# Kernel optimization log

Hardware: AMD Instinct MI355X
Metric: run time of the kernel (lower is better)

Reference implementation:

```python
import jax, jax.numpy as jnp
import numpy as np

EMB = 1024
NH = 8
HD = EMB // NH
EPS = 1e-6


def setup_inputs() -> dict:
    key = jax.random.key(0)
    ks = jax.random.split(key, 6)
    B, S = 2, 2048
    q = jax.random.normal(ks[0], (B, S, EMB), jnp.float32)
    k = jax.random.normal(ks[1], (B, S, EMB), jnp.float32)
    v = jax.random.normal(ks[2], (B, S, EMB), jnp.float32)
    # gate Dense params: input dim 3*EMB (concat of q,k,v), output NH
    igate_kernel = jax.random.normal(ks[3], (3 * EMB, NH), jnp.float32) * 0.02
    igate_bias = jax.random.normal(ks[4], (NH,), jnp.float32) * 0.1
    fgate_kernel = jax.random.normal(ks[5], (3 * EMB, NH), jnp.float32) * 0.02
    fgate_bias = jnp.linspace(3.0, 6.0, NH).astype(jnp.float32)  # bias_linspace_init
    return dict(q=q, k=k, v=v, igate_kernel=igate_kernel, igate_bias=igate_bias,
                fgate_kernel=fgate_kernel, fgate_bias=fgate_bias)


def _mlstm_head(q, k, v, ig, fg):
    # q,k,v: (S, DH); ig, fg: (S, 1) gate preactivations for this head
    S, DH = q.shape
    log_fg = jax.nn.log_sigmoid(fg)                                   # (S,1)
    cs = jnp.concatenate([jnp.zeros((1, 1), q.dtype),
                          jnp.cumsum(log_fg, axis=0)], axis=0)        # (S+1,1)
    fg_mat_full = cs - cs.T                                           # (S+1,S+1): cumsum_i - cumsum_j
    ltr = jnp.tril(jnp.ones((S, S), bool))
    log_fg_matrix = jnp.where(ltr, fg_mat_full[1:, 1:], -jnp.inf)     # causal decay
    log_D = log_fg_matrix + ig.T                                      # (S,S)
    max_log_D = jnp.max(log_D, axis=-1, keepdims=True)                # row-wise stabilizer
    D = jnp.exp(log_D - max_log_D)
    qk = q @ (k.T / jnp.sqrt(jnp.asarray(DH, q.dtype)))               # (S,S)
    C = qk * D
    normalizer = jnp.maximum(jnp.abs(C.sum(-1, keepdims=True)), jnp.exp(-max_log_D))
    return (C / (normalizer + EPS)) @ v                               # (S,DH)


def reference(q, k, v, igate_kernel, igate_bias, fgate_kernel, fgate_bias):
    B, S, H = q.shape
    x = jnp.concatenate([q, k, v], axis=-1)                           # (B,S,3H)
    ig = x @ igate_kernel + igate_bias                                # (B,S,NH)
    fg = x @ fgate_kernel + fgate_bias                                # (B,S,NH)
    qh = q.reshape(B, S, NH, HD).swapaxes(1, 2)                       # (B,NH,S,DH)
    kh = k.reshape(B, S, NH, HD).swapaxes(1, 2)
    vh = v.reshape(B, S, NH, HD).swapaxes(1, 2)
    igp = ig.swapaxes(1, 2)[..., None]                                # (B,NH,S,1)
    fgp = fg.swapaxes(1, 2)[..., None]
    h = jax.vmap(jax.vmap(_mlstm_head))(qh, kh, vh, igp, fgp)         # (B,NH,S,DH)
    # RMSNorm over head_dim (last axis), computed in fp32
    hf = h.astype(jnp.float32)
    h = (hf * jax.lax.rsqrt(jnp.mean(jnp.square(hf), axis=-1, keepdims=True) + 1e-6)).astype(h.dtype)
    return h.swapaxes(1, 2).reshape(B, S, H)
```

## Files before the change

kernel.cpp:

```cpp
#include <hip/hip_runtime.h>

#define S_LEN 2048
#define EMB_D 1024
#define QK_SCALE 0.08838834764831845f
#define RS128 11.313708498984761f
#define LOG2E 1.4426950408889634f

typedef _Float16 f16;
typedef f16 f16x8 __attribute__((ext_vector_type(8)));
typedef float f32x4 __attribute__((ext_vector_type(4)));
typedef unsigned short ushort_t;

typedef const __attribute__((address_space(1))) void gvoid;
typedef __attribute__((address_space(3))) void lvoid;

__device__ __forceinline__ ushort_t f2h(float x) {
    return __builtin_bit_cast(ushort_t, (f16)x);
}
__device__ __forceinline__ unsigned pk2h(float a, float b) {
    return __builtin_bit_cast(unsigned, __builtin_amdgcn_cvt_pkrtz(a, b));
}
__device__ __forceinline__ void gl_lds(const void* g, void* l) {
    __builtin_amdgcn_global_load_lds((gvoid*)g, (lvoid*)l, 16, 0, 0);
}

__global__ __launch_bounds__(256) void ktransW(const float* __restrict__ igk,
                                               const float* __restrict__ fgk,
                                               ushort_t* __restrict__ Wf) {
    int gid = blockIdx.x * 256 + threadIdx.x;
    int ks_g = gid >> 6, lane = gid & 63;
    int n = lane & 15, lg = lane >> 4;
    int src = ks_g >> 5, rem = ks_g & 31;
    int hemb = rem >> 2, ks = rem & 3;
    int e0 = src * 1024 + hemb * 128 + ks * 32 + lg * 8;
    float scale = (src == 0) ? RS128 : 1.0f;
    const float* col = (n < 8) ? igk : fgk;
    int nn = n & 7;
    union { ushort_t u[8]; uint4 v4; } P;
    #pragma unroll
    for (int e = 0; e < 8; ++e) P.u[e] = f2h(col[(size_t)(e0 + e) * 8 + nn] * scale);
    *(uint4*)((char*)Wf + ks_g * 1024 + lane * 16) = P.v4;
}

__global__ __launch_bounds__(256) void kprep(const float* __restrict__ q,
                                             const float* __restrict__ k,
                                             const float* __restrict__ v,
                                             const ushort_t* __restrict__ Wf,
                                             const float* __restrict__ igb,
                                             const float* __restrict__ fgb,
                                             ushort_t* __restrict__ Qf,
                                             ushort_t* __restrict__ Kf,
                                             ushort_t* __restrict__ Vt,
                                             float* __restrict__ igp_t,
                                             float* __restrict__ fgp_t) {
    __shared__ __align__(16) ushort_t xs[3 * 8 * 16 * 128];
    __shared__ __align__(16) float red[4][64][4];
    const int blk = blockIdx.x;
    const int b = blk >> 7, strip = blk & 127;
    const int s0 = strip * 16;
    const int tile = strip >> 2, subrow = (strip & 3) * 16;
    const int t = threadIdx.x;
    const int w = t >> 6, lane = t & 63;
    const int ll = lane & 15, lg = lane >> 4;

    #pragma unroll
    for (int src = 0; src < 3; ++src) {
        const float* sp = (src == 0 ? q : src == 1 ? k : v) + ((size_t)b * S_LEN + s0) * EMB_D;
        float scale = (src == 0) ? QK_SCALE : 1.0f;
        #pragma unroll
        for (int i = 0; i < 16; ++i) {
            int f = i * 256 + t;
            int r = f >> 8, c4 = f & 255;
            int col = c4 * 4;
            float4 x = *(const float4*)(sp + (size_t)r * EMB_D + col);
            ushort4 H;
            H.x = f2h(x.x * scale); H.y = f2h(x.y * scale);
            H.z = f2h(x.z * scale); H.w = f2h(x.w * scale);
            int hh = col >> 7, d0 = col & 127;
            *(ushort4*)((char*)xs + ((((src * 8 + hh) * 16 + r) * 256 + d0 * 2) ^ ((r & 7) << 4))) = H;
            if (src < 2) {
                char* dst = (char*)(src ? Kf : Qf) + ((size_t)(b * 8 + hh) * 32 + tile) * 16384;
                *(ushort4*)(dst + (((subrow + r) * 256 + d0 * 2) ^ ((r & 7) << 4))) = H;
            }
        }
    }
    __syncthreads();
    #pragma unroll
    for (int it = 0; it < 8; ++it) {
        int item = it * 256 + t;
        int d = item & 127, jo = (item >> 7) & 1, hh = item >> 8;
        union { ushort_t u[8]; uint4 v4; } P;
        #pragma unroll
        for (int e = 0; e < 8; ++e) {
            int r = jo * 8 + e;
            P.u[e] = *(const ushort_t*)((const char*)xs
                       + ((((16 + hh) * 16 + r) * 256 + d * 2) ^ ((r & 7) << 4)));
        }
        char* vd = (char*)Vt + ((size_t)(b * 8 + hh) * 32 + tile) * 16384
                 + ((strip & 3) * 2 + jo) * 2048 + d * 16;
        *(uint4*)vd = P.v4;
    }
    f32x4 acc = {0.f, 0.f, 0.f, 0.f};
    for (int ri = w * 6; ri < w * 6 + 6; ++ri) {
        int src = ri >> 3, hemb = ri & 7;
        #pragma unroll
        for (int ks = 0; ks < 4; ++ks) {
            f16x8 af = *(const f16x8*)((const char*)xs
                        + ((((src * 8 + hemb) * 16 + ll) * 256 + ks * 64 + lg * 16) ^ ((ll & 7) << 4)));
            f16x8 bf = *(const f16x8*)((const char*)Wf + (src * 32 + hemb * 4 + ks) * 1024 + lane * 16);
            acc = __builtin_amdgcn_mfma_f32_16x16x32_f16(af, bf, acc, 0, 0, 0);
        }
    }
    *(f32x4*)&red[w][lane][0] = acc;
    __syncthreads();
    if (w == 0) {
        f32x4 o2 = acc;
        #pragma unroll
        for (int ww = 1; ww < 4; ++ww) o2 += *(const f32x4*)&red[ww][lane][0];
        float bias = (ll < 8) ? igb[ll] : fgb[ll - 8];
        float* dst = (ll < 8) ? igp_t : fgp_t;
        size_t ob = (size_t)(b * 8 + (ll & 7)) * S_LEN + s0 + lg * 4;
        #pragma unroll
        for (int r = 0; r < 4; ++r) dst[ob + r] = o2[r] + bias;
    }
}

__global__ __launch_bounds__(64) void kscan(const float* __restrict__ igp_t,
                                            const float* __restrict__ fgp_t,
                                            float* __restrict__ a_w,
                                            float* __restrict__ pm_w,
                                            float* __restrict__ nf_w) {
    const int bh = blockIdx.x;
    const int l = threadIdx.x;
    const int base = bh * S_LEN + l * 32;
    float lf[32];
    #pragma unroll
    for (int i = 0; i < 8; ++i) {
        float4 fg = *(const float4*)(fgp_t + base + i * 4);
        float* p = &lf[i * 4];
        p[0] = fminf(fg.x, 0.f) - log1pf(__expf(-fabsf(fg.x)));
        p[1] = fminf(fg.y, 0.f) - log1pf(__expf(-fabsf(fg.y)));
        p[2] = fminf(fg.z, 0.f) - log1pf(__expf(-fabsf(fg.z)));
        p[3] = fminf(fg.w, 0.f) - log1pf(__expf(-fabsf(fg.w)));
    }
    #pragma unroll
    for (int i = 1; i < 32; ++i) lf[i] += lf[i - 1];
    float tot = lf[31];
    #pragma unroll
    for (int d = 1; d < 64; d <<= 1) {
        float n = __shfl_up(tot, d, 64);
        if (l >= d) tot += n;
    }
    float excl = tot - lf[31];
    float cs[32], a[32];
    #pragma unroll
    for (int i = 0; i < 8; ++i) {
        float4 ig = *(const float4*)(igp_t + base + i * 4);
        float iv[4] = {ig.x, ig.y, ig.z, ig.w};
        #pragma unroll
        for (int e = 0; e < 4; ++e) {
            int idx = i * 4 + e;
            cs[idx] = excl + lf[idx];
            a[idx] = iv[e] - cs[idx];
            a_w[base + idx] = a[idx] * LOG2E;
        }
    }
    float am[32];
    am[0] = a[0];
    #pragma unroll
    for (int i = 1; i < 32; ++i) am[i] = fmaxf(am[i - 1], a[i]);
    float mtot = am[31];
    #pragma unroll
    for (int d = 1; d < 64; d <<= 1) {
        float n = __shfl_up(mtot, d, 64);
        if (l >= d) mtot = fmaxf(mtot, n);
    }
    float exm = __shfl_up(mtot, 1, 64);
    if (l == 0) exm = -INFINITY;
    #pragma unroll
    for (int i = 0; i < 32; ++i) {
        float pmv = fmaxf(exm, am[i]);
        pm_w[base + i] = pmv * LOG2E;
        nf_w[base + i] = __expf(-(cs[i] + pmv));
    }
}

__global__ __launch_bounds__(512) void kmain(const ushort_t* __restrict__ Qf,
                                             const ushort_t* __restrict__ Kf,
                                             const ushort_t* __restrict__ Vt,
                                             const float* __restrict__ a_w,
                                             const float* __restrict__ pm_w,
                                             const float* __restrict__ nf_w,
                                             float* __restrict__ out) {
    __shared__ __align__(16) ushort_t Kbuf[2][2][8192];
    __shared__ __align__(16) ushort_t Vbuf[2][2][8192];
    __shared__ __align__(16) ushort_t Csh[2][4096];
    __shared__ float redL[2][2][64];

    const int blk = blockIdx.x;
    const int bh = blk & 15;
    const int pair = blk >> 4;
    const int b = bh >> 3, h = bh & 7;
    const int t = threadIdx.x;
    const int w = t >> 6, lane = t & 63;
    const int g = w >> 2, wl = w & 3;
    const int wr = wl >> 1, wc = wl & 1;
    const int lg = lane >> 4, ll = lane & 15;
    const int sw = (ll & 7) << 4;

    const char* q_b = (const char*)Qf + (size_t)bh * 524288;
    const char* k_b = (const char*)Kf + (size_t)bh * 524288;
    const char* v_b = (const char*)Vt + (size_t)bh * 524288;
    const float* aw = a_w + bh * S_LEN;

    float* accX = (float*)&Kbuf[0][0][0];
    float* rsX  = (float*)&Csh[0][0];

    for (int half = 0; half < 2; ++half) {
        const int rt = half ? (31 - pair) : pair;
        const int row0 = rt * 64;
        const int T0h = (rt >> 1) + 1;
        const int T1h = (rt >= 1) ? (((rt - 1) >> 1) + 1) : 0;
        const int Tg  = g ? T1h : T0h;
        const int Nint = (2 * T1h + 1 > 2 * T0h) ? (2 * T1h + 1) : (2 * T0h);
        __syncthreads();

        const char* qt = q_b + (size_t)rt * 16384;
        f16x8 qf[2][4];
        #pragma unroll
        for (int ib = 0; ib < 2; ++ib) {
            int row = 32 * wr + 16 * ib + ll;
            #pragma unroll
            for (int kk = 0; kk < 4; ++kk)
                qf[ib][kk] = *(const f16x8*)(qt + ((row * 256 + lg * 16 + kk * 64) ^ ((row & 7) << 4)));
        }
        float pm2[2];
        #pragma unroll
        for (int ib = 0; ib < 2; ++ib)
            pm2[ib] = pm_w[bh * S_LEN + row0 + 32 * wr + 16 * ib + ll];

        f32x4 avA[2] = {{0.f,0.f,0.f,0.f},{0.f,0.f,0.f,0.f}};
        f32x4 avB[2] = {{0.f,0.f,0.f,0.f},{0.f,0.f,0.f,0.f}};
        if (Tg > 0) {
            const char* kt = k_b + (size_t)g * 16384;
            const char* vt = v_b + (size_t)g * 16384;
            #pragma unroll
            for (int i = 0; i < 4; ++i) {
                int o = (wl * 4 + i) * 1024 + lane * 16;
                gl_lds(kt + o, (char*)&Kbuf[g][0][0] + o);
                gl_lds(vt + o, (char*)&Vbuf[g][0][0] + o);
            }
            #pragma unroll
            for (int jb = 0; jb < 2; ++jb)
                avA[jb] = *(const f32x4*)(aw + g * 64 + 32 * wc + 16 * jb + 4 * lg);
        }
        asm volatile("s_waitcnt vmcnt(0)" ::: "memory");
        __builtin_amdgcn_s_barrier();

        f32x4 zero4 = {0.f, 0.f, 0.f, 0.f};
        f32x4 accO[2][4];
        #pragma unroll
        for (int ib = 0; ib < 2; ++ib)
            #pragma unroll
            for (int vf = 0; vf < 4; ++vf) accO[ib][vf] = zero4;
        float rs[2] = {0.f, 0.f};

        for (int i = 0; i < Nint; ++i) {
            const int d = i - g;
            const bool isQK = (d >= 0) && ((d & 1) == 0) && ((d >> 1) < Tg);
            const bool isPV = (d >= 1) && ((d & 1) == 1) && (((d - 1) >> 1) < Tg);
            if (isQK) {
                const int tt = d >> 1;
                const int ct = 2 * tt + g;
                if (tt + 1 < Tg) {
                    const int nct = ct + 2;
                    const char* kt = k_b + (size_t)nct * 16384;
                    const char* vt = v_b + (size_t)nct * 16384;
                    const int pn = (tt + 1) & 1;
                    #pragma unroll
                    for (int ii = 0; ii < 4; ++ii) {
                        int o = (wl * 4 + ii) * 1024 + lane * 16;
                        gl_lds(kt + o, (char*)&Kbuf[g][pn][0] + o);
                        gl_lds(vt + o, (char*)&Vbuf[g][pn][0] + o);
                    }
                    if ((tt + 1) & 1) {
                        #pragma unroll
                        for (int jb = 0; jb < 2; ++jb)
                            avB[jb] = *(const f32x4*)(aw + nct * 64 + 32 * wc + 16 * jb + 4 * lg);
                    } else {
                        #pragma unroll
                        for (int jb = 0; jb < 2; ++jb)
                            avA[jb] = *(const f32x4*)(aw + nct * 64 + 32 * wc + 16 * jb + 4 * lg);
                    }
                }
                const char* kl = (const char*)&Kbuf[g][tt & 1][0];
                f32x4 accST[2][2];
                accST[0][0] = zero4; accST[0][1] = zero4;
                accST[1][0] = zero4; accST[1][1] = zero4;
                __builtin_amdgcn_s_setprio(1);
                #pragma unroll
                for (int kk = 0; kk < 4; ++kk) {
                    f16x8 kf0 = *(const f16x8*)(kl + (((32 * wc + ll) * 256 + lg * 16 + kk * 64) ^ sw));
                    f16x8 kf1 = *(const f16x8*)(kl + (((32 * wc + 16 + ll) * 256 + lg * 16 + kk * 64) ^ sw));
                    accST[0][0] = __builtin_amdgcn_mfma_f32_16x16x32_f16(kf0, qf[0][kk], accST[0][0], 0, 0, 0);
                    accST[0][1] = __builtin_amdgcn_mfma_f32_16x16x32_f16(kf0, qf[1][kk], accST[0][1], 0, 0, 0);
                    accST[1][0] = __builtin_amdgcn_mfma_f32_16x16x32_f16(kf1, qf[0][kk], accST[1][0], 0, 0, 0);
                    accST[1][1] = __builtin_amdgcn_mfma_f32_16x16x32_f16(kf1, qf[1][kk], accST[1][1], 0, 0, 0);
                }
                __builtin_amdgcn_s_setprio(0);
                const bool diag = (ct == rt);
                #pragma unroll
                for (int jb = 0; jb < 2; ++jb) {
                    f32x4 av;
                    #pragma unroll
                    for (int r = 0; r < 4; ++r) av[r] = (tt & 1) ? avB[jb][r] : avA[jb][r];
                    #pragma unroll
                    for (int ib = 0; ib < 2; ++ib) {
                        int il = 32 * wr + 16 * ib + ll;
                        float cv[4];
                        #pragma unroll
                        for (int r = 0; r < 4; ++r) {
                            int jl = 32 * wc + 16 * jb + 4 * lg + r;
                            float x = accST[jb][ib][r] * exp2f(av[r] - pm2[ib]);
                            if (diag && jl > il) x = 0.f;
                            rs[ib] += x;
                            cv[r] = x;
                        }
                        int off = (il * 128 + (32 * wc + 16 * jb + 4 * lg) * 2) ^ ((il & 7) << 4);
                        uint2 pk2; pk2.x = pk2h(cv[0], cv[1]); pk2.y = pk2h(cv[2], cv[3]);
                        *(uint2*)((char*)&Csh[g][0] + off) = pk2;
                    }
                }
                asm volatile("s_waitcnt lgkmcnt(0)" ::: "memory");
            }
            if (isPV) {
                const int tp = (d - 1) >> 1;
                const char* vl = (const char*)&Vbuf[g][tp & 1][0];
                __builtin_amdgcn_s_setprio(1);
                #pragma unroll
                for (int kk = 0; kk < 2; ++kk)
                    #pragma unroll
                    for (int ib = 0; ib < 2; ++ib) {
                        int rowA = 32 * wr + 16 * ib + ll;
                        f16x8 pa = *(const f16x8*)((const char*)&Csh[g][0]
                                                   + ((rowA * 128 + lg * 16 + kk * 64) ^ ((rowA & 7) << 4)));
                        #pragma unroll
                        for (int vf = 0; vf < 4; ++vf) {
                            f16x8 vb2 = *(const f16x8*)(vl + (kk * 4 + lg) * 2048
                                                        + (64 * wc + 16 * vf + ll) * 16);
                            accO[ib][vf] = __builtin_amdgcn_mfma_f32_16x16x32_f16(pa, vb2, accO[ib][vf], 0, 0, 0);
                        }
                    }
                __builtin_amdgcn_s_setprio(0);
                asm volatile("s_waitcnt vmcnt(0)" ::: "memory");
            }
            __builtin_amdgcn_s_barrier();
        }

        __syncthreads();
        const int li = wl * 64 + lane;
        const int lsw = (li & 7) << 2;
        if (g == 1) {
            #pragma unroll
            for (int ib = 0; ib < 2; ++ib)
                #pragma unroll
                for (int vf = 0; vf < 4; ++vf)
                    *(f32x4*)&accX[(li * 32 + (ib * 4 + vf) * 4) ^ lsw] = accO[ib][vf];
            rsX[li * 2 + 0] = rs[0];
            rsX[li * 2 + 1] = rs[1];
        }
        __syncthreads();
        if (g == 0) {
            #pragma unroll
            for (int ib = 0; ib < 2; ++ib)
                #pragma unroll
                for (int vf = 0; vf < 4; ++vf)
                    accO[ib][vf] += *(const f32x4*)&accX[(li * 32 + (ib * 4 + vf) * 4) ^ lsw];
            rs[0] += rsX[li * 2 + 0];
            rs[1] += rsX[li * 2 + 1];
            #pragma unroll
            for (int ib = 0; ib < 2; ++ib) {
                rs[ib] += __shfl_xor(rs[ib], 16);
                rs[ib] += __shfl_xor(rs[ib], 32);
            }
            if (lg == 0) {
                redL[0][wc][32 * wr + ll] = rs[0];
                redL[0][wc][32 * wr + 16 + ll] = rs[1];
            }
        }
        __syncthreads();
        if (g == 0) {
            float invn[2][4];
            #pragma unroll
            for (int ib = 0; ib < 2; ++ib)
                #pragma unroll
                for (int r = 0; r < 4; ++r) {
                    int il = 32 * wr + 16 * ib + 4 * lg + r;
                    float tot = redL[0][0][il] + redL[0][1][il];
                    float nf = nf_w[bh * S_LEN + row0 + il];
                    invn[ib][r] = 1.0f / (fmaxf(fabsf(tot), nf) + 1e-6f);
                }
            float ssq[2][4] = {{0.f, 0.f, 0.f, 0.f}, {0.f, 0.f, 0.f, 0.f}};
            #pragma unroll
            for (int ib = 0; ib < 2; ++ib)
                #pragma unroll
                for (int vf = 0; vf < 4; ++vf)
                    #pragma unroll
                    for (int r = 0; r < 4; ++r) {
                        float hv = accO[ib][vf][r] * invn[ib][r];
                        ssq[ib][r] += hv * hv;
                    }
            #pragma unroll
            for (int m = 1; m < 16; m <<= 1)
                #pragma unroll
                for (int ib = 0; ib < 2; ++ib)
                    #pragma unroll
                    for (int r = 0; r < 4; ++r) ssq[ib][r] += __shfl_xor(ssq[ib][r], m);
            if (ll == 0) {
                #pragma unroll
                for (int ib = 0; ib < 2; ++ib)
                    #pragma unroll
                    for (int r = 0; r < 4; ++r)
                        redL[1][wc][32 * wr + 16 * ib + 4 * lg + r] = ssq[ib][r];
            }
            __builtin_amdgcn_s_barrier();
            float* ob = out + ((size_t)b * S_LEN + row0) * EMB_D + h * 128;
            #pragma unroll
            for (int ib = 0; ib < 2; ++ib)
                #pragma unroll
                for (int r = 0; r < 4; ++r) {
                    int il = 32 * wr + 16 * ib + 4 * lg + r;
                    float sst = redL[1][0][il] + redL[1][1][il];
                    float scl = rsqrtf(sst * (1.0f / 128.0f) + 1e-6f) * invn[ib][r];
                    #pragma unroll
                    for (int vf = 0; vf < 4; ++vf) {
                        int d2 = 64 * wc + 16 * vf + ll;
                        ob[(size_t)il * EMB_D + d2] = accO[ib][vf][r] * scl;
                    }
                }
        } else {
            __builtin_amdgcn_s_barrier();
        }
    }
}

extern "C" void kernel_launch(void* const* d_in, const int* in_sizes, int n_in,
                              void* d_out, int out_size, void* d_ws, size_t ws_size,
                              hipStream_t stream) {
    const float* q   = (const float*)d_in[0];
    const float* k   = (const float*)d_in[1];
    const float* v   = (const float*)d_in[2];
    const float* igk = (const float*)d_in[3];
    const float* igb = (const float*)d_in[4];
    const float* fgk = (const float*)d_in[5];
    const float* fgb = (const float*)d_in[6];
    float* out = (float*)d_out;

    char* W = (char*)d_ws;
    ushort_t* Wf   = (ushort_t*)(W);
    float* igp_t   = (float*)(W + 98304);
    float* fgp_t   = (float*)(W + 229376);
    float* a_w     = (float*)(W + 360448);
    float* pm_w    = (float*)(W + 491520);
    float* nf_w    = (float*)(W + 622592);
    ushort_t* Qf   = (ushort_t*)(W + 753664);
    ushort_t* Kf   = (ushort_t*)(W + 753664 + 1 * 8388608ull);
    ushort_t* Vt   = (ushort_t*)(W + 753664 + 2 * 8388608ull);

    ktransW<<<24, 256, 0, stream>>>(igk, fgk, Wf);
    kprep<<<256, 256, 0, stream>>>(q, k, v, Wf, igb, fgb, Qf, Kf, Vt, igp_t, fgp_t);
    kscan<<<16, 64, 0, stream>>>(igp_t, fgp_t, a_w, pm_w, nf_w);
    kmain<<<256, 512, 0, stream>>>(Qf, Kf, Vt, a_w, pm_w, nf_w, out);
}
```

Measured before the change: 90.76 us.

## Split kmain into one row tile per block without key-split groups

Replaces the two-group key-split, staggered QK/PV pipeline (512-thread blocks each processing two row tiles) with 256-thread blocks that each handle a single row tile over all causal key tiles. This removes the cross-group accumulator reduction through LDS and halves shared memory per block, and launches twice as many blocks with heavy tiles scheduled first. In exchange it loses the intra-block overlap of one group's QK with the other's PV, and the longest rows now run a longer serial chain per block.

```diff
diff --git a/kernel.cpp b/kernel.cpp
--- a/kernel.cpp
+++ b/kernel.cpp
@@ -185,26 +185,27 @@
     }
 }
 
-__global__ __launch_bounds__(512) void kmain(const ushort_t* __restrict__ Qf,
+__global__ __launch_bounds__(256) void kmain(const ushort_t* __restrict__ Qf,
                                              const ushort_t* __restrict__ Kf,
                                              const ushort_t* __restrict__ Vt,
                                              const float* __restrict__ a_w,
                                              const float* __restrict__ pm_w,
                                              const float* __restrict__ nf_w,
                                              float* __restrict__ out) {
-    __shared__ __align__(16) ushort_t Kbuf[2][2][8192];
-    __shared__ __align__(16) ushort_t Vbuf[2][2][8192];
-    __shared__ __align__(16) ushort_t Csh[2][4096];
+    __shared__ __align__(16) ushort_t Kbuf[2][8192];
+    __shared__ __align__(16) ushort_t Vbuf[2][8192];
+    __shared__ __align__(16) ushort_t Csh[4096];
     __shared__ float redL[2][2][64];
 
     const int blk = blockIdx.x;
     const int bh = blk & 15;
-    const int pair = blk >> 4;
+    const int jj = (blk >> 4) & 15;
+    const int rt = (blk < 256) ? (31 - jj) : jj;
+    const int row0 = rt * 64;
     const int b = bh >> 3, h = bh & 7;
     const int t = threadIdx.x;
     const int w = t >> 6, lane = t & 63;
-    const int g = w >> 2, wl = w & 3;
-    const int wr = wl >> 1, wc = wl & 1;
+    const int wr = w >> 1, wc = w & 1;
     const int lg = lane >> 4, ll = lane & 15;
     const int sw = (ll & 7) << 4;
 
@@ -213,235 +214,189 @@
     const char* v_b = (const char*)Vt + (size_t)bh * 524288;
     const float* aw = a_w + bh * S_LEN;
 
-    float* accX = (float*)&Kbuf[0][0][0];
-    float* rsX  = (float*)&Csh[0][0];
-
-    for (int half = 0; half < 2; ++half) {
-        const int rt = half ? (31 - pair) : pair;
-        const int row0 = rt * 64;
-        const int T0h = (rt >> 1) + 1;
-        const int T1h = (rt >= 1) ? (((rt - 1) >> 1) + 1) : 0;
-        const int Tg  = g ? T1h : T0h;
-        const int Nint = (2 * T1h + 1 > 2 * T0h) ? (2 * T1h + 1) : (2 * T0h);
-        __syncthreads();
-
-        const char* qt = q_b + (size_t)rt * 16384;
-        f16x8 qf[2][4];
-        #pragma unroll
-        for (int ib = 0; ib < 2; ++ib) {
-            int row = 32 * wr + 16 * ib + ll;
-            #pragma unroll
-            for (int kk = 0; kk < 4; ++kk)
-                qf[ib][kk] = *(const f16x8*)(qt + ((row * 256 + lg * 16 + kk * 64) ^ ((row & 7) << 4)));
-        }
-        float pm2[2];
-        #pragma unroll
-        for (int ib = 0; ib < 2; ++ib)
-            pm2[ib] = pm_w[bh * S_LEN + row0 + 32 * wr + 16 * ib + ll];
-
-        f32x4 avA[2] = {{0.f,0.f,0.f,0.f},{0.f,0.f,0.f,0.f}};
-        f32x4 avB[2] = {{0.f,0.f,0.f,0.f},{0.f,0.f,0.f,0.f}};
-        if (Tg > 0) {
-            const char* kt = k_b + (size_t)g * 16384;
-            const char* vt = v_b + (size_t)g * 16384;
+    const char* qt = q_b + (size_t)rt * 16384;
+    f16x8 qf[2][4];
+    #pragma unroll
+    for (int ib = 0; ib < 2; ++ib) {
+        int row = 32 * wr + 16 * ib + ll;
+        #pragma unroll
+        for (int kk = 0; kk < 4; ++kk)
+            qf[ib][kk] = *(const f16x8*)(qt + ((row * 256 + lg * 16 + kk * 64) ^ ((row & 7) << 4)));
+    }
+    float pm2[2];
+    #pragma unroll
+    for (int ib = 0; ib < 2; ++ib)
+        pm2[ib] = pm_w[bh * S_LEN + row0 + 32 * wr + 16 * ib + ll];
+
+    f32x4 avA[2], avB[2];
+    {
+        const char* kt = k_b;
+        const char* vt = v_b;
+        #pragma unroll
+        for (int i = 0; i < 4; ++i) {
+            int o = (w * 4 + i) * 1024 + lane * 16;
+            gl_lds(kt + o, (char*)&Kbuf[0][0] + o);
+            gl_lds(vt + o, (char*)&Vbuf[0][0] + o);
+        }
+        #pragma unroll
+        for (int jb = 0; jb < 2; ++jb)
+            avA[jb] = *(const f32x4*)(aw + 32 * wc + 16 * jb + 4 * lg);
+        avB[0] = avA[0]; avB[1] = avA[1];
+    }
+    asm volatile("s_waitcnt vmcnt(0)" ::: "memory");
+    __builtin_amdgcn_s_barrier();
+
+    f32x4 zero4 = {0.f, 0.f, 0.f, 0.f};
+    f32x4 accO[2][4];
+    #pragma unroll
+    for (int ib = 0; ib < 2; ++ib)
+        #pragma unroll
+        for (int vf = 0; vf < 4; ++vf) accO[ib][vf] = zero4;
+    float rs[2] = {0.f, 0.f};
+
+    for (int ct = 0; ct <= rt; ++ct) {
+        const int p = ct & 1;
+        if (ct < rt) {
+            const int nct = ct + 1;
+            const char* kt = k_b + (size_t)nct * 16384;
+            const char* vt = v_b + (size_t)nct * 16384;
             #pragma unroll
             for (int i = 0; i < 4; ++i) {
-                int o = (wl * 4 + i) * 1024 + lane * 16;
-                gl_lds(kt + o, (char*)&Kbuf[g][0][0] + o);
-                gl_lds(vt + o, (char*)&Vbuf[g][0][0] + o);
-            }
-            #pragma unroll
-            for (int jb = 0; jb < 2; ++jb)
-                avA[jb] = *(const f32x4*)(aw + g * 64 + 32 * wc + 16 * jb + 4 * lg);
+                int o = (w * 4 + i) * 1024 + lane * 16;
+                gl_lds(kt + o, (char*)&Kbuf[p ^ 1][0] + o);
+                gl_lds(vt + o, (char*)&Vbuf[p ^ 1][0] + o);
+            }
+            if (p == 0) {
+                #pragma unroll
+                for (int jb = 0; jb < 2; ++jb)
+                    avB[jb] = *(const f32x4*)(aw + nct * 64 + 32 * wc + 16 * jb + 4 * lg);
+            } else {
+                #pragma unroll
+                for (int jb = 0; jb < 2; ++jb)
+                    avA[jb] = *(const f32x4*)(aw + nct * 64 + 32 * wc + 16 * jb + 4 * lg);
+            }
+        }
+        const char* kl = (const char*)&Kbuf[p][0];
+        f32x4 accST[2][2];
+        accST[0][0] = zero4; accST[0][1] = zero4;
+        accST[1][0] = zero4; accST[1][1] = zero4;
+        __builtin_amdgcn_s_setprio(1);
+        #pragma unroll
+        for (int kk = 0; kk < 4; ++kk) {
+            f16x8 kf0 = *(const f16x8*)(kl + (((32 * wc + ll) * 256 + lg * 16 + kk * 64) ^ sw));
+            f16x8 kf1 = *(const f16x8*)(kl + (((32 * wc + 16 + ll) * 256 + lg * 16 + kk * 64) ^ sw));
+            accST[0][0] = __builtin_amdgcn_mfma_f32_16x16x32_f16(kf0, qf[0][kk], accST[0][0], 0, 0, 0);
+            accST[0][1] = __builtin_amdgcn_mfma_f32_16x16x32_f16(kf0, qf[1][kk], accST[0][1], 0, 0, 0);
+            accST[1][0] = __builtin_amdgcn_mfma_f32_16x16x32_f16(kf1, qf[0][kk], accST[1][0], 0, 0, 0);
+            accST[1][1] = __builtin_amdgcn_mfma_f32_16x16x32_f16(kf1, qf[1][kk], accST[1][1], 0, 0, 0);
+        }
+        __builtin_amdgcn_s_setprio(0);
+        const bool diag = (ct == rt);
+        #pragma unroll
+        for (int jb = 0; jb < 2; ++jb) {
+            f32x4 av;
+            #pragma unroll
+            for (int r = 0; r < 4; ++r) av[r] = (p == 0) ? avA[jb][r] : avB[jb][r];
+            #pragma unroll
+            for (int ib = 0; ib < 2; ++ib) {
+                int il = 32 * wr + 16 * ib + ll;
+                float cv[4];
+                #pragma unroll
+                for (int r = 0; r < 4; ++r) {
+                    int jl = 32 * wc + 16 * jb + 4 * lg + r;
+                    float x = accST[jb][ib][r] * exp2f(av[r] - pm2[ib]);
+                    if (diag && jl > il) x = 0.f;
+                    rs[ib] += x;
+                    cv[r] = x;
+                }
+                int off = (il * 128 + (32 * wc + 16 * jb + 4 * lg) * 2) ^ ((il & 7) << 4);
+                uint2 pk2; pk2.x = pk2h(cv[0], cv[1]); pk2.y = pk2h(cv[2], cv[3]);
+                *(uint2*)((char*)&Csh[0] + off) = pk2;
+            }
+        }
+        asm volatile("s_waitcnt lgkmcnt(0)" ::: "memory");
+        __builtin_amdgcn_s_barrier();
+        {
+            const char* vl = (const char*)&Vbuf[p][0];
+            __builtin_amdgcn_s_setprio(1);
+            #pragma unroll
+            for (int kk = 0; kk < 2; ++kk)
+                #pragma unroll
+                for (int ib = 0; ib < 2; ++ib) {
+                    int rowA = 32 * wr + 16 * ib + ll;
+                    f16x8 pa = *(const f16x8*)((const char*)&Csh[0]
+                                               + ((rowA * 128 + lg * 16 + kk * 64) ^ ((rowA & 7) << 4)));
+                    #pragma unroll
+                    for (int vf = 0; vf < 4; ++vf) {
+                        f16x8 vb2 = *(const f16x8*)(vl + (kk * 4 + lg) * 2048
+                                                    + (64 * wc + 16 * vf + ll) * 16);
+                        accO[ib][vf] = __builtin_amdgcn_mfma_f32_16x16x32_f16(pa, vb2, accO[ib][vf], 0, 0, 0);
+                    }
+                }
+            __builtin_amdgcn_s_setprio(0);
         }
         asm volatile("s_waitcnt vmcnt(0)" ::: "memory");
         __builtin_amdgcn_s_barrier();
-
-        f32x4 zero4 = {0.f, 0.f, 0.f, 0.f};
-        f32x4 accO[2][4];
+    }
+
+    #pragma unroll
+    for (int ib = 0; ib < 2; ++ib) {
+        rs[ib] += __shfl_xor(rs[ib], 16);
+        rs[ib] += __shfl_xor(rs[ib], 32);
+    }
+    if (lg == 0) {
+        redL[0][wc][32 * wr + ll] = rs[0];
+        redL[0][wc][32 * wr + 16 + ll] = rs[1];
+    }
+    __syncthreads();
+    float invn[2][4];
+    #pragma unroll
+    for (int ib = 0; ib < 2; ++ib)
+        #pragma unroll
+        for (int r = 0; r < 4; ++r) {
+            int il = 32 * wr + 16 * ib + 4 * lg + r;
+            float tot = redL[0][0][il] + redL[0][1][il];
+            float nf = nf_w[bh * S_LEN + row0 + il];
+            invn[ib][r] = 1.0f / (fmaxf(fabsf(tot), nf) + 1e-6f);
+        }
+    float ssq[2][4] = {{0.f, 0.f, 0.f, 0.f}, {0.f, 0.f, 0.f, 0.f}};
+    #pragma unroll
+    for (int ib = 0; ib < 2; ++ib)
+        #pragma unroll
+        for (int vf = 0; vf < 4; ++vf)
+            #pragma unroll
+            for (int r = 0; r < 4; ++r) {
+                float hv = accO[ib][vf][r] * invn[ib][r];
+                ssq[ib][r] += hv * hv;
+            }
+    #pragma unroll
+    for (int m = 1; m < 16; m <<= 1)
         #pragma unroll
         for (int ib = 0; ib < 2; ++ib)
             #pragma unroll
-            for (int vf = 0; vf < 4; ++vf) accO[ib][vf] = zero4;
-        float rs[2] = {0.f, 0.f};
-
-        for (int i = 0; i < Nint; ++i) {
-            const int d = i - g;
-            const bool isQK = (d >= 0) && ((d & 1) == 0) && ((d >> 1) < Tg);
-            const bool isPV = (d >= 1) && ((d & 1) == 1) && (((d - 1) >> 1) < Tg);
-            if (isQK) {
-                const int tt = d >> 1;
-                const int ct = 2 * tt + g;
-                if (tt + 1 < Tg) {
-                    const int nct = ct + 2;
-                    const char* kt = k_b + (size_t)nct * 16384;
-                    const char* vt = v_b + (size_t)nct * 16384;
-                    const int pn = (tt + 1) & 1;
-                    #pragma unroll
-                    for (int ii = 0; ii < 4; ++ii) {
-                        int o = (wl * 4 + ii) * 1024 + lane * 16;
-                        gl_lds(kt + o, (char*)&Kbuf[g][pn][0] + o);
-                        gl_lds(vt + o, (char*)&Vbuf[g][pn][0] + o);
-                    }
-                    if ((tt + 1) & 1) {
-                        #pragma unroll
-                        for (int jb = 0; jb < 2; ++jb)
-                            avB[jb] = *(const f32x4*)(aw + nct * 64 + 32 * wc + 16 * jb + 4 * lg);
-                    } else {
-                        #pragma unroll
-                        for (int jb = 0; jb < 2; ++jb)
-                            avA[jb] = *(const f32x4*)(aw + nct * 64 + 32 * wc + 16 * jb + 4 * lg);
-                    }
-                }
-                const char* kl = (const char*)&Kbuf[g][tt & 1][0];
-                f32x4 accST[2][2];
-                accST[0][0] = zero4; accST[0][1] = zero4;
-                accST[1][0] = zero4; accST[1][1] = zero4;
-                __builtin_amdgcn_s_setprio(1);
-                #pragma unroll
-                for (int kk = 0; kk < 4; ++kk) {
-                    f16x8 kf0 = *(const f16x8*)(kl + (((32 * wc + ll) * 256 + lg * 16 + kk * 64) ^ sw));
-                    f16x8 kf1 = *(const f16x8*)(kl + (((32 * wc + 16 + ll) * 256 + lg * 16 + kk * 64) ^ sw));
-                    accST[0][0] = __builtin_amdgcn_mfma_f32_16x16x32_f16(kf0, qf[0][kk], accST[0][0], 0, 0, 0);
-                    accST[0][1] = __builtin_amdgcn_mfma_f32_16x16x32_f16(kf0, qf[1][kk], accST[0][1], 0, 0, 0);
-                    accST[1][0] = __builtin_amdgcn_mfma_f32_16x16x32_f16(kf1, qf[0][kk], accST[1][0], 0, 0, 0);
-                    accST[1][1] = __builtin_amdgcn_mfma_f32_16x16x32_f16(kf1, qf[1][kk], accST[1][1], 0, 0, 0);
-                }
-                __builtin_amdgcn_s_setprio(0);
-                const bool diag = (ct == rt);
-                #pragma unroll
-                for (int jb = 0; jb < 2; ++jb) {
-                    f32x4 av;
-                    #pragma unroll
-                    for (int r = 0; r < 4; ++r) av[r] = (tt & 1) ? avB[jb][r] : avA[jb][r];
-                    #pragma unroll
-                    for (int ib = 0; ib < 2; ++ib) {
-                        int il = 32 * wr + 16 * ib + ll;
-                        float cv[4];
-                        #pragma unroll
-                        for (int r = 0; r < 4; ++r) {
-                            int jl = 32 * wc + 16 * jb + 4 * lg + r;
-                            float x = accST[jb][ib][r] * exp2f(av[r] - pm2[ib]);
-                            if (diag && jl > il) x = 0.f;
-                            rs[ib] += x;
-                            cv[r] = x;
-                        }
-                        int off = (il * 128 + (32 * wc + 16 * jb + 4 * lg) * 2) ^ ((il & 7) << 4);
-                        uint2 pk2; pk2.x = pk2h(cv[0], cv[1]); pk2.y = pk2h(cv[2], cv[3]);
-                        *(uint2*)((char*)&Csh[g][0] + off) = pk2;
-                    }
-                }
-                asm volatile("s_waitcnt lgkmcnt(0)" ::: "memory");
-            }
-            if (isPV) {
-                const int tp = (d - 1) >> 1;
-                const char* vl = (const char*)&Vbuf[g][tp & 1][0];
-                __builtin_amdgcn_s_setprio(1);
-                #pragma unroll
-                for (int kk = 0; kk < 2; ++kk)
-                    #pragma unroll
-                    for (int ib = 0; ib < 2; ++ib) {
-                        int rowA = 32 * wr + 16 * ib + ll;
-                        f16x8 pa = *(const f16x8*)((const char*)&Csh[g][0]
-                                                   + ((rowA * 128 + lg * 16 + kk * 64) ^ ((rowA & 7) << 4)));
-                        #pragma unroll
-                        for (int vf = 0; vf < 4; ++vf) {
-                            f16x8 vb2 = *(const f16x8*)(vl + (kk * 4 + lg) * 2048
-                                                        + (64 * wc + 16 * vf + ll) * 16);
-                            accO[ib][vf] = __builtin_amdgcn_mfma_f32_16x16x32_f16(pa, vb2, accO[ib][vf], 0, 0, 0);
-                        }
-                    }
-                __builtin_amdgcn_s_setprio(0);
-                asm volatile("s_waitcnt vmcnt(0)" ::: "memory");
-            }
-            __builtin_amdgcn_s_barrier();
-        }
-
-        __syncthreads();
-        const int li = wl * 64 + lane;
-        const int lsw = (li & 7) << 2;
-        if (g == 1) {
-            #pragma unroll
-            for (int ib = 0; ib < 2; ++ib)
-                #pragma unroll
-                for (int vf = 0; vf < 4; ++vf)
-                    *(f32x4*)&accX[(li * 32 + (ib * 4 + vf) * 4) ^ lsw] = accO[ib][vf];
-            rsX[li * 2 + 0] = rs[0];
-            rsX[li * 2 + 1] = rs[1];
-        }
-        __syncthreads();
-        if (g == 0) {
-            #pragma unroll
-            for (int ib = 0; ib < 2; ++ib)
-                #pragma unroll
-                for (int vf = 0; vf < 4; ++vf)
-                    accO[ib][vf] += *(const f32x4*)&accX[(li * 32 + (ib * 4 + vf) * 4) ^ lsw];
-            rs[0] += rsX[li * 2 + 0];
-            rs[1] += rsX[li * 2 + 1];
-            #pragma unroll
-            for (int ib = 0; ib < 2; ++ib) {
-                rs[ib] += __shfl_xor(rs[ib], 16);
-                rs[ib] += __shfl_xor(rs[ib], 32);
-            }
-            if (lg == 0) {
-                redL[0][wc][32 * wr + ll] = rs[0];
-                redL[0][wc][32 * wr + 16 + ll] = rs[1];
-            }
-        }
-        __syncthreads();
-        if (g == 0) {
-            float invn[2][4];
-            #pragma unroll
-            for (int ib = 0; ib < 2; ++ib)
-                #pragma unroll
-                for (int r = 0; r < 4; ++r) {
-                    int il = 32 * wr + 16 * ib + 4 * lg + r;
-                    float tot = redL[0][0][il] + redL[0][1][il];
-                    float nf = nf_w[bh * S_LEN + row0 + il];
-                    invn[ib][r] = 1.0f / (fmaxf(fabsf(tot), nf) + 1e-6f);
-                }
-            float ssq[2][4] = {{0.f, 0.f, 0.f, 0.f}, {0.f, 0.f, 0.f, 0.f}};
-            #pragma unroll
-            for (int ib = 0; ib < 2; ++ib)
-                #pragma unroll
-                for (int vf = 0; vf < 4; ++vf)
-                    #pragma unroll
-                    for (int r = 0; r < 4; ++r) {
-                        float hv = accO[ib][vf][r] * invn[ib][r];
-                        ssq[ib][r] += hv * hv;
-                    }
-            #pragma unroll
-            for (int m = 1; m < 16; m <<= 1)
-                #pragma unroll
-                for (int ib = 0; ib < 2; ++ib)
-                    #pragma unroll
-                    for (int r = 0; r < 4; ++r) ssq[ib][r] += __shfl_xor(ssq[ib][r], m);
-            if (ll == 0) {
-                #pragma unroll
-                for (int ib = 0; ib < 2; ++ib)
-                    #pragma unroll
-                    for (int r = 0; r < 4; ++r)
-                        redL[1][wc][32 * wr + 16 * ib + 4 * lg + r] = ssq[ib][r];
-            }
-            __builtin_amdgcn_s_barrier();
-            float* ob = out + ((size_t)b * S_LEN + row0) * EMB_D + h * 128;
-            #pragma unroll
-            for (int ib = 0; ib < 2; ++ib)
-                #pragma unroll
-                for (int r = 0; r < 4; ++r) {
-                    int il = 32 * wr + 16 * ib + 4 * lg + r;
-                    float sst = redL[1][0][il] + redL[1][1][il];
-                    float scl = rsqrtf(sst * (1.0f / 128.0f) + 1e-6f) * invn[ib][r];
-                    #pragma unroll
-                    for (int vf = 0; vf < 4; ++vf) {
-                        int d2 = 64 * wc + 16 * vf + ll;
-                        ob[(size_t)il * EMB_D + d2] = accO[ib][vf][r] * scl;
-                    }
-                }
-        } else {
-            __builtin_amdgcn_s_barrier();
-        }
-    }
+            for (int r = 0; r < 4; ++r) ssq[ib][r] += __shfl_xor(ssq[ib][r], m);
+    if (ll == 0) {
+        #pragma unroll
+        for (int ib = 0; ib < 2; ++ib)
+            #pragma unroll
+            for (int r = 0; r < 4; ++r)
+                redL[1][wc][32 * wr + 16 * ib + 4 * lg + r] = ssq[ib][r];
+    }
+    __syncthreads();
+    float* ob = out + ((size_t)b * S_LEN + row0) * EMB_D + h * 128;
+    #pragma unroll
+    for (int ib = 0; ib < 2; ++ib)
+        #pragma unroll
+        for (int r = 0; r < 4; ++r) {
+            int il = 32 * wr + 16 * ib + 4 * lg + r;
+            float sst = redL[1][0][il] + redL[1][1][il];
+            float scl = rsqrtf(sst * (1.0f / 128.0f) + 1e-6f) * invn[ib][r];
+            #pragma unroll
+            for (int vf = 0; vf < 4; ++vf) {
+                int d2 = 64 * wc + 16 * vf + ll;
+                ob[(size_t)il * EMB_D + d2] = accO[ib][vf][r] * scl;
+            }
+        }
 }
 
 extern "C" void kernel_launch(void* const* d_in, const int* in_sizes, int n_in,
@@ -470,5 +425,5 @@
     ktransW<<<24, 256, 0, stream>>>(igk, fgk, Wf);
     kprep<<<256, 256, 0, stream>>>(q, k, v, Wf, igb, fgb, Qf, Kf, Vt, igp_t, fgp_t);
     kscan<<<16, 64, 0, stream>>>(igp_t, fgp_t, a_w, pm_w, nf_w);
-    kmain<<<256, 512, 0, stream>>>(Qf, Kf, Vt, a_w, pm_w, nf_w, out);
-}
+    kmain<<<512, 256, 0, stream>>>(Qf, Kf, Vt, a_w, pm_w, nf_w, out);
+}
```

New measurement: 90.19 us. Within noise of the previous version (-0.6%).
